# Performance work log

Hardware: AMD Instinct MI355X
Metric: run time of the kernel (lower is better)

Reference implementation:

```python
import jax, jax.numpy as jnp
import numpy as np

B, T, L = 4096, 26, 4      # batch, num sparse tables, bag size (multi-hot)
N_ROWS, M = 100000, 64     # rows per table, embedding dim
LN_BOT = [13, 512, 256, 64]
LN_TOP = [415, 512, 256, 1]


def _mlp_params(key, ln):
    Ws, bs = [], []
    for i in range(len(ln) - 1):
        n, m = ln[i], ln[i + 1]
        key, k1, k2 = jax.random.split(key, 3)
        Ws.append(jax.random.normal(k1, (m, n), jnp.float32) * np.sqrt(2.0 / (m + n)))
        bs.append(jax.random.normal(k2, (m,), jnp.float32) * np.sqrt(1.0 / m))
    return Ws, bs


def setup_inputs() -> dict:
    key = jax.random.key(0)
    k_dense, k_idx, k_emb, k_bot, k_top = jax.random.split(key, 5)
    dense_x = jax.random.normal(k_dense, (B, LN_BOT[0]), jnp.float32)
    sparse_idx = jax.random.randint(k_idx, (B, T, L), 0, N_ROWS, jnp.int64 if jax.config.jax_enable_x64 else jnp.int32)
    # per-table uniform init U(-1/sqrt(n), 1/sqrt(n)); all tables same size -> stacked
    bound = np.sqrt(1.0 / N_ROWS)
    emb_tables = jax.random.uniform(k_emb, (T, N_ROWS, M), jnp.float32, -bound, bound)
    bw, bb = _mlp_params(k_bot, LN_BOT)
    tw, tb = _mlp_params(k_top, LN_TOP)
    return {
        "dense_x": dense_x, "sparse_idx": sparse_idx, "emb_tables": emb_tables,
        "bot_W0": bw[0], "bot_b0": bb[0], "bot_W1": bw[1], "bot_b1": bb[1],
        "bot_W2": bw[2], "bot_b2": bb[2],
        "top_W0": tw[0], "top_b0": tb[0], "top_W1": tw[1], "top_b1": tb[1],
        "top_W2": tw[2], "top_b2": tb[2],
    }


def _dlrm_forward(dense_x, sparse_idx, emb_tables, bot, top):
    # bottom MLP (all ReLU; sigmoid_layer index not hit for bottom)
    x = dense_x
    for W, b in bot:
        x = jax.nn.relu(x @ W.T + b)                       # [B, 64] at the end
    # apply_emb: per-table EmbeddingBag(mode='sum'): gather L rows, sum-pool
    # emb_tables: [T, N, M], sparse_idx: [B, T, L] -> E: [B, T, M]
    E = jax.vmap(lambda tab, ix: tab[ix].sum(axis=1), in_axes=(0, 1), out_axes=1)(
        emb_tables, sparse_idx)
    # dot interaction: concat bottom output with pooled embeddings
    Tcat = jnp.concatenate([x[:, None, :], E], axis=1)     # [B, T+1, M]
    Z = jnp.einsum("bim,bjm->bij", Tcat, Tcat)             # [B, T+1, T+1]
    li, lj = np.tril_indices(T + 1, k=-1)                  # strictly lower triangle
    Zflat = Z[:, li, lj]                                   # [B, (T+1)T/2]
    R = jnp.concatenate([x, Zflat], axis=1)                # [B, 415]
    # top MLP: ReLU hidden, Sigmoid on last layer
    h = R
    for i, (W, b) in enumerate(top):
        h = h @ W.T + b
        h = jax.nn.sigmoid(h) if i == len(top) - 1 else jax.nn.relu(h)
    return h                                               # [B, 1]


def reference(dense_x, sparse_idx, emb_tables,
              bot_W0, bot_b0, bot_W1, bot_b1, bot_W2, bot_b2,
              top_W0, top_b0, top_W1, top_b1, top_W2, top_b2):
    bot = [(bot_W0, bot_b0), (bot_W1, bot_b1), (bot_W2, bot_b2)]
    top = [(top_W0, top_b0), (top_W1, top_b1), (top_W2, top_b2)]
    return _dlrm_forward(dense_x, sparse_idx, emb_tables, bot, top)
```

## Files before the change

kernel.cpp:

```cpp
#include <hip/hip_runtime.h>
#include <hip/hip_bf16.h>
#include <cstddef>
#include <cstdint>

#define BATCH 4096
#define TT 26
#define LL 4
#define NROWS 100000
#define MM 64
#define RSTR 512

typedef __attribute__((ext_vector_type(8))) short bf16x8;
typedef __attribute__((ext_vector_type(4))) float f32x4;
typedef __attribute__((ext_vector_type(16))) float f32x16;

#define AS1 __attribute__((address_space(1)))
#define AS3 __attribute__((address_space(3)))

__device__ __forceinline__ void gload_lds16(const void* g, void* l) {
    __builtin_amdgcn_global_load_lds((const AS1 unsigned int*)g,
                                     (AS3 unsigned int*)l, 16, 0, 0);
}

__device__ __forceinline__ float bu2f(unsigned short u) {
    unsigned int x = (unsigned int)u << 16;
    float f; __builtin_memcpy(&f, &x, 4); return f;
}

#define CONV_BLOCKS 2112
__global__ __launch_bounds__(256) void prep_kernel(
    const float* __restrict__ dense, const float* __restrict__ bw0,
    const float* __restrict__ bb0,
    const float* __restrict__ bw1, const float* __restrict__ bw2,
    const float* __restrict__ tw0, const float* __restrict__ tw1,
    __hip_bfloat16* __restrict__ x1,
    __hip_bfloat16* __restrict__ bw1b, __hip_bfloat16* __restrict__ bw2b,
    __hip_bfloat16* __restrict__ tw0b, __hip_bfloat16* __restrict__ tw1b)
{
    __shared__ float xr[13];
    if (blockIdx.x < CONV_BLOCKS) {
        int i = blockIdx.x * 256 + threadIdx.x;
        if (i < 131072) {
            bw1b[i] = __float2bfloat16(bw1[i]);
        } else if (i < 147456) {
            int j = i - 131072; bw2b[j] = __float2bfloat16(bw2[j]);
        } else if (i < 409600) {
            int j = i - 147456; int n = j >> 9, k = j & 511;
            tw0b[j] = __float2bfloat16(k < 415 ? tw0[n * 415 + k] : 0.f);
        } else {
            int j = i - 409600; tw1b[j] = __float2bfloat16(tw1[j]);
        }
        return;
    }
    int b = blockIdx.x - CONV_BLOCKS;
    if (threadIdx.x < 13) xr[threadIdx.x] = dense[b * 13 + threadIdx.x];
    __syncthreads();
    for (int j = threadIdx.x; j < 512; j += 256) {
        const float* w = bw0 + j * 13;
        float s = bb0[j];
#pragma unroll
        for (int k = 0; k < 13; k++) s = fmaf(xr[k], w[k], s);
        x1[(size_t)b * 512 + j] = __float2bfloat16(fmaxf(s, 0.f));
    }
}

template<int KK, int ACT>
__global__ __launch_bounds__(256) void gemm_fullk(
    const __hip_bfloat16* __restrict__ A,
    const __hip_bfloat16* __restrict__ W,
    const float* __restrict__ bias,
    __hip_bfloat16* __restrict__ C, int ldc)
{
    constexpr int HS   = KK / 2;
    constexpr int CPRH = KK / 16;
    constexpr int NI   = (64 * CPRH) / 256;
    __shared__ __align__(16) short As0[64 * HS];
    __shared__ __align__(16) short As1[64 * HS];
    __shared__ __align__(16) short Bs0[64 * HS];
    __shared__ __align__(16) short Bs1[64 * HS];

    const int tid  = threadIdx.x;
    const int lane = tid & 63;
    const int wid  = tid >> 6;
    const int wr   = wid >> 1, wc = wid & 1;

    const char* Ab = (const char*)A + (size_t)blockIdx.x * (64 * KK * 2);
    const char* Wb = (const char*)W + (size_t)blockIdx.y * (64 * KK * 2);

    auto stage = [&](const char* Gb, short* Ls, int h) {
#pragma unroll
        for (int j = 0; j < NI; j++) {
            int ci  = j * 256 + tid;
            int row = ci / CPRH;
            int cb  = (ci & (CPRH - 1)) * 16;
            int src = row * (2 * KK) + h * KK + (cb ^ ((row & 7) << 4));
            gload_lds16(Gb + src, (char*)Ls + row * KK + cb);
        }
    };
    stage(Ab, As0, 0); stage(Wb, Bs0, 0);
    stage(Ab, As1, 1); stage(Wb, Bs1, 1);

    const int frow = lane & 15;
    const int fkb  = (lane >> 4) * 16;
    const int xr   = (frow & 7) << 4;
    const int oA0  = (wr * 32 + frow) * KK;
    const int oA1  = oA0 + 16 * KK;
    const int oB0  = (wc * 32 + frow) * KK;
    const int oB1  = oB0 + 16 * KK;

    f32x4 acc[2][2] = {};

    auto compute = [&](const short* Ah, const short* Bh) {
#pragma unroll
        for (int ks = 0; ks < KK / 64; ks++) {
            int pc = (ks * 64 + fkb) ^ xr;
            bf16x8 a0 = *(const bf16x8*)((const char*)Ah + oA0 + pc);
            bf16x8 a1 = *(const bf16x8*)((const char*)Ah + oA1 + pc);
            bf16x8 b0 = *(const bf16x8*)((const char*)Bh + oB0 + pc);
            bf16x8 b1 = *(const bf16x8*)((const char*)Bh + oB1 + pc);
            acc[0][0] = __builtin_amdgcn_mfma_f32_16x16x32_bf16(a0, b0, acc[0][0], 0, 0, 0);
            acc[0][1] = __builtin_amdgcn_mfma_f32_16x16x32_bf16(a0, b1, acc[0][1], 0, 0, 0);
            acc[1][0] = __builtin_amdgcn_mfma_f32_16x16x32_bf16(a1, b0, acc[1][0], 0, 0, 0);
            acc[1][1] = __builtin_amdgcn_mfma_f32_16x16x32_bf16(a1, b1, acc[1][1], 0, 0, 0);
        }
    };

    asm volatile("s_waitcnt vmcnt(%0)" :: "i"(2 * NI) : "memory");
    __builtin_amdgcn_sched_barrier(0);
    __builtin_amdgcn_s_barrier();
    __builtin_amdgcn_sched_barrier(0);
    compute(As0, Bs0);
    asm volatile("s_waitcnt vmcnt(0)" ::: "memory");
    __builtin_amdgcn_sched_barrier(0);
    __builtin_amdgcn_s_barrier();
    __builtin_amdgcn_sched_barrier(0);
    compute(As1, Bs1);

    const int col0 = blockIdx.y * 64 + wc * 32 + (lane & 15);
    const int row0 = blockIdx.x * 64 + wr * 32 + (lane >> 4) * 4;
    float bias_n0 = bias[col0];
    float bias_n1 = bias[col0 + 16];
#pragma unroll
    for (int mi = 0; mi < 2; mi++) {
#pragma unroll
        for (int j = 0; j < 4; j++) {
            int row = row0 + mi * 16 + j;
            float v0 = acc[mi][0][j] + bias_n0;
            float v1 = acc[mi][1][j] + bias_n1;
            if (ACT == 1) { v0 = fmaxf(v0, 0.f); v1 = fmaxf(v1, 0.f); }
            C[(size_t)row * ldc + col0]      = __float2bfloat16(v0);
            C[(size_t)row * ldc + col0 + 16] = __float2bfloat16(v1);
        }
    }
}

__global__ __launch_bounds__(256) void embed_interact_kernel(
    const int* __restrict__ idx, const float* __restrict__ emb,
    __hip_bfloat16* __restrict__ R)
{
    __shared__ __align__(16) short T[32 * 64];
    __shared__ int sidx[TT * LL];
    const int b = blockIdx.x;
    const int tid = threadIdx.x;
    const int lane = tid & 63;
    const int w = tid >> 6;

    if (tid < TT * LL) sidx[tid] = idx[(size_t)b * (TT * LL) + tid];
    for (int i = tid; i < 5 * 64; i += 256) {
        int r = 27 + (i >> 6), l = i & 63;
        *(short*)((char*)T + r * 128 + ((l * 2) ^ ((r & 7) << 4))) = 0;
    }
    __syncthreads();

    float v[7][4];
#pragma unroll
    for (int rr = 0; rr < 7; rr++) {
        const int r = rr * 4 + w;
        if (r == 0) {
            v[rr][0] = __bfloat162float(R[(size_t)b * RSTR + lane]);
            v[rr][1] = 0.f; v[rr][2] = 0.f; v[rr][3] = 0.f;
        } else if (r < 27) {
            const int t = r - 1;
            const float* tab = emb + (size_t)t * NROWS * MM + lane;
#pragma unroll
            for (int l = 0; l < LL; l++)
                v[rr][l] = tab[(size_t)sidx[t * LL + l] * MM];
        }
    }
#pragma unroll
    for (int rr = 0; rr < 7; rr++) {
        const int r = rr * 4 + w;
        if (r < 27) {
            float s = v[rr][0] + v[rr][1] + v[rr][2] + v[rr][3];
            __hip_bfloat16 hv = __float2bfloat16(s);
            *(short*)((char*)T + r * 128 + ((lane * 2) ^ ((r & 7) << 4))) = *(short*)&hv;
        }
    }
    __syncthreads();

    __hip_bfloat16* Rb = R + (size_t)b * RSTR;
    if (w == 1) {
        Rb[415 + lane] = __float2bfloat16(0.f);
        if (lane < 33) Rb[479 + lane] = __float2bfloat16(0.f);
    }
    if (w == 0) {
        f32x16 acc = {};
#pragma unroll
        for (int m = 0; m < 4; m++) {
            int byteoff = (lane & 31) * 128 +
                          ((m * 32 + (lane >> 5) * 16) ^ ((lane & 7) << 4));
            bf16x8 f = *(const bf16x8*)((const char*)T + byteoff);
            acc = __builtin_amdgcn_mfma_f32_32x32x16_bf16(f, f, acc, 0, 0, 0);
        }
        const int col = lane & 31;
#pragma unroll
        for (int q = 0; q < 4; q++) {
#pragma unroll
            for (int j = 0; j < 4; j++) {
                int row = j + 8 * q + 4 * (lane >> 5);
                if (row < 27 && col < row)
                    Rb[64 + row * (row - 1) / 2 + col] = __float2bfloat16(acc[q * 4 + j]);
            }
        }
    }
}

__global__ __launch_bounds__(256) void top2_kernel(
    const __hip_bfloat16* __restrict__ h, const float* __restrict__ W,
    const float* __restrict__ bias, float* __restrict__ out)
{
    __shared__ float ws[256];
    int tid = threadIdx.x;
    ws[tid] = W[tid];
    __syncthreads();
    int b = blockIdx.x * 4 + (tid >> 6);
    int lane = tid & 63;
    const unsigned short* hb = (const unsigned short*)(h + (size_t)b * 256);
    ushort4 hv = *(const ushort4*)&hb[lane * 4];
    float4 wv = *(const float4*)&ws[lane * 4];
    float s = bu2f(hv.x) * wv.x + bu2f(hv.y) * wv.y + bu2f(hv.z) * wv.z + bu2f(hv.w) * wv.w;
#pragma unroll
    for (int off = 32; off >= 1; off >>= 1)
        s += __shfl_xor(s, off, 64);
    if (lane == 0) {
        float v = s + bias[0];
        out[b] = 1.0f / (1.0f + expf(-v));
    }
}

extern "C" void kernel_launch(void* const* d_in, const int* in_sizes, int n_in,
                              void* d_out, int out_size, void* d_ws, size_t ws_size,
                              hipStream_t stream) {
    const float* dense = (const float*)d_in[0];
    const int*   sidx  = (const int*)d_in[1];
    const float* emb   = (const float*)d_in[2];
    const float* bw0   = (const float*)d_in[3];
    const float* bb0   = (const float*)d_in[4];
    const float* bw1   = (const float*)d_in[5];
    const float* bb1   = (const float*)d_in[6];
    const float* bw2   = (const float*)d_in[7];
    const float* bb2   = (const float*)d_in[8];
    const float* tw0   = (const float*)d_in[9];
    const float* tb0   = (const float*)d_in[10];
    const float* tw1   = (const float*)d_in[11];
    const float* tb1   = (const float*)d_in[12];
    const float* tw2   = (const float*)d_in[13];
    const float* tb2   = (const float*)d_in[14];
    float* out = (float*)d_out;

    char* wsb = (char*)d_ws;
    __hip_bfloat16* x1   = (__hip_bfloat16*)(wsb);
    __hip_bfloat16* x2   = (__hip_bfloat16*)(wsb + (4u << 20));
    __hip_bfloat16* R    = (__hip_bfloat16*)(wsb + (8u << 20));
    __hip_bfloat16* h1   = (__hip_bfloat16*)(wsb + (12u << 20));
    __hip_bfloat16* h2   = (__hip_bfloat16*)(wsb + (16u << 20));
    __hip_bfloat16* bw1b = (__hip_bfloat16*)(wsb + (18u << 20));
    __hip_bfloat16* bw2b = bw1b + 131072;
    __hip_bfloat16* tw0b = bw2b + 16384;
    __hip_bfloat16* tw1b = tw0b + 262144;

    prep_kernel<<<CONV_BLOCKS + BATCH, 256, 0, stream>>>(
        dense, bw0, bb0, bw1, bw2, tw0, tw1, x1, bw1b, bw2b, tw0b, tw1b);

    gemm_fullk<512, 1><<<dim3(64, 4), 256, 0, stream>>>(x1, bw1b, bb1, x2, 256);

    gemm_fullk<256, 1><<<dim3(64, 1), 256, 0, stream>>>(x2, bw2b, bb2, R, RSTR);

    embed_interact_kernel<<<BATCH, 256, 0, stream>>>(sidx, emb, R);

    gemm_fullk<512, 1><<<dim3(64, 8), 256, 0, stream>>>(R, tw0b, tb0, h1, 512);

    gemm_fullk<512, 1><<<dim3(64, 4), 256, 0, stream>>>(h1, tw1b, tb1, h2, 256);

    top2_kernel<<<BATCH / 4, 256, 0, stream>>>(h2, tw2, tb2, out);
}
```

Baseline: 54.66 us.

## Fuse bottom MLP into one kernel, move embedding gather into prep kernel

The embedding gather now runs inside the weight-conversion prep kernel and writes pooled bf16 embeddings to a workspace buffer. All three bottom-MLP layers are fused into one kernel that processes 16 rows per block, keeping activations in LDS and using MFMA, which removes two GEMM launches and the x1/x2 round trips. A separate interaction kernel then handles four samples per block, one per wave. The aim is fewer launches and less intermediate traffic, at the cost of an extra E buffer round trip and a bottom MLP that runs on only 256 blocks.

After: 61.00 us. +11.6%, slower.

```diff
diff --git a/kernel.cpp b/kernel.cpp
--- a/kernel.cpp
+++ b/kernel.cpp
@@ -27,19 +27,19 @@
     float f; __builtin_memcpy(&f, &x, 4); return f;
 }
 
-#define CONV_BLOCKS 2112
-__global__ __launch_bounds__(256) void prep_kernel(
-    const float* __restrict__ dense, const float* __restrict__ bw0,
-    const float* __restrict__ bb0,
+#define CONVB 2112
+__global__ __launch_bounds__(256) void gather_conv_kernel(
+    const int* __restrict__ idx, const float* __restrict__ emb,
     const float* __restrict__ bw1, const float* __restrict__ bw2,
     const float* __restrict__ tw0, const float* __restrict__ tw1,
-    __hip_bfloat16* __restrict__ x1,
     __hip_bfloat16* __restrict__ bw1b, __hip_bfloat16* __restrict__ bw2b,
-    __hip_bfloat16* __restrict__ tw0b, __hip_bfloat16* __restrict__ tw1b)
-{
-    __shared__ float xr[13];
-    if (blockIdx.x < CONV_BLOCKS) {
-        int i = blockIdx.x * 256 + threadIdx.x;
+    __hip_bfloat16* __restrict__ tw0b, __hip_bfloat16* __restrict__ tw1b,
+    unsigned short* __restrict__ E)
+{
+    __shared__ int sidx[TT * LL];
+    const int tid = threadIdx.x;
+    if (blockIdx.x < CONVB) {
+        int i = blockIdx.x * 256 + tid;
         if (i < 131072) {
             bw1b[i] = __float2bfloat16(bw1[i]);
         } else if (i < 147456) {
@@ -52,16 +52,170 @@
         }
         return;
     }
-    int b = blockIdx.x - CONV_BLOCKS;
-    if (threadIdx.x < 13) xr[threadIdx.x] = dense[b * 13 + threadIdx.x];
-    __syncthreads();
-    for (int j = threadIdx.x; j < 512; j += 256) {
-        const float* w = bw0 + j * 13;
-        float s = bb0[j];
-#pragma unroll
-        for (int k = 0; k < 13; k++) s = fmaf(xr[k], w[k], s);
-        x1[(size_t)b * 512 + j] = __float2bfloat16(fmaxf(s, 0.f));
-    }
+    const int b = blockIdx.x - CONVB;
+    const int lane = tid & 63;
+    const int w = tid >> 6;
+    if (tid < TT * LL) sidx[tid] = idx[(size_t)b * (TT * LL) + tid];
+    __syncthreads();
+
+    float v[7][4];
+#pragma unroll
+    for (int rr = 0; rr < 7; rr++) {
+        int t = rr * 4 + w;
+        if (t < TT) {
+            const float* tab = emb + (size_t)t * NROWS * MM + lane;
+#pragma unroll
+            for (int l = 0; l < LL; l++)
+                v[rr][l] = tab[(size_t)sidx[t * LL + l] * MM];
+        }
+    }
+#pragma unroll
+    for (int rr = 0; rr < 7; rr++) {
+        int t = rr * 4 + w;
+        if (t < TT) {
+            float s = v[rr][0] + v[rr][1] + v[rr][2] + v[rr][3];
+            __hip_bfloat16 hv = __float2bfloat16(s);
+            E[(size_t)b * (TT * MM) + t * MM + lane] = *(unsigned short*)&hv;
+        }
+    }
+}
+
+__global__ __launch_bounds__(256) void bottom_mlp_kernel(
+    const float* __restrict__ dense, const float* __restrict__ bw0,
+    const float* __restrict__ bb0,
+    const __hip_bfloat16* __restrict__ w1b, const float* __restrict__ bb1,
+    const __hip_bfloat16* __restrict__ w2b, const float* __restrict__ bb2,
+    __hip_bfloat16* __restrict__ R)
+{
+    __shared__ float W0f[512 * 13];
+    __shared__ float dL[16 * 13];
+    __shared__ __align__(16) char x1L[16 * 1024];
+    __shared__ __align__(16) char x2L[16 * 512];
+    const int tid = threadIdx.x;
+    const int lane = tid & 63;
+    const int w = tid >> 6;
+    const int b0 = blockIdx.x * 16;
+
+    for (int i = tid; i < 512 * 13; i += 256) W0f[i] = bw0[i];
+    if (tid < 208) dL[tid] = dense[(size_t)b0 * 13 + tid];
+    __syncthreads();
+
+    {
+        const int m = tid & 15;
+        float dv[13];
+#pragma unroll
+        for (int k = 0; k < 13; k++) dv[k] = dL[m * 13 + k];
+#pragma unroll
+        for (int j = 0; j < 32; j++) {
+            int n = (tid >> 4) + j * 16;
+            float s = bb0[n];
+#pragma unroll
+            for (int k = 0; k < 13; k++) s = fmaf(dv[k], W0f[n * 13 + k], s);
+            __hip_bfloat16 hv = __float2bfloat16(fmaxf(s, 0.f));
+            *(short*)(x1L + m * 1024 + ((n * 2) ^ ((m & 7) << 4))) = *(short*)&hv;
+        }
+    }
+    __syncthreads();
+
+    const int fr = lane & 15;
+    const int fh = lane >> 4;
+
+    {
+        f32x4 acc1[4] = {};
+#pragma unroll
+        for (int kf = 0; kf < 16; kf++) {
+            bf16x8 af = *(const bf16x8*)(x1L + fr * 1024 + ((kf * 64 + fh * 16) ^ ((fr & 7) << 4)));
+#pragma unroll
+            for (int nf = 0; nf < 4; nf++) {
+                int n = w * 64 + nf * 16 + fr;
+                bf16x8 bf = *(const bf16x8*)((const short*)w1b + (size_t)n * 512 + kf * 32 + fh * 8);
+                acc1[nf] = __builtin_amdgcn_mfma_f32_16x16x32_bf16(af, bf, acc1[nf], 0, 0, 0);
+            }
+        }
+#pragma unroll
+        for (int nf = 0; nf < 4; nf++) {
+            int n = w * 64 + nf * 16 + fr;
+            float bias = bb1[n];
+#pragma unroll
+            for (int j = 0; j < 4; j++) {
+                int m = fh * 4 + j;
+                __hip_bfloat16 hv = __float2bfloat16(fmaxf(acc1[nf][j] + bias, 0.f));
+                *(short*)(x2L + m * 512 + ((n * 2) ^ ((m & 7) << 4))) = *(short*)&hv;
+            }
+        }
+    }
+    __syncthreads();
+
+    {
+        f32x4 acc2 = {};
+#pragma unroll
+        for (int kf = 0; kf < 8; kf++) {
+            bf16x8 af = *(const bf16x8*)(x2L + fr * 512 + ((kf * 64 + fh * 16) ^ ((fr & 7) << 4)));
+            bf16x8 bf = *(const bf16x8*)((const short*)w2b + (size_t)(w * 16 + fr) * 256 + kf * 32 + fh * 8);
+            acc2 = __builtin_amdgcn_mfma_f32_16x16x32_bf16(af, bf, acc2, 0, 0, 0);
+        }
+        int col = w * 16 + fr;
+        float bias = bb2[col];
+#pragma unroll
+        for (int j = 0; j < 4; j++) {
+            int m = fh * 4 + j;
+            R[(size_t)(b0 + m) * RSTR + col] = __float2bfloat16(fmaxf(acc2[j] + bias, 0.f));
+        }
+    }
+}
+
+__global__ __launch_bounds__(256) void interact_kernel(
+    const unsigned short* __restrict__ E, __hip_bfloat16* __restrict__ R)
+{
+    __shared__ __align__(16) char T[4][32 * 128];
+    const int tid = threadIdx.x;
+    const int lane = tid & 63;
+    const int w = tid >> 6;
+    const int b = blockIdx.x * 4 + w;
+    char* Tw = T[w];
+    const unsigned short* Eb = E + (size_t)b * (TT * MM);
+    const unsigned short* Xb = (const unsigned short*)R + (size_t)b * RSTR;
+
+#pragma unroll
+    for (int i = 0; i < 7; i++) {
+        int id = i * 64 + lane;
+        if (id < 432) {
+            int r = id >> 4, c4 = (id & 15) * 4;
+            const unsigned short* src = (r == 0) ? (Xb + c4) : (Eb + (r - 1) * 64 + c4);
+            ushort4 val = *(const ushort4*)src;
+            *(ushort4*)(Tw + r * 128 + ((c4 * 2) ^ ((r & 7) << 4))) = val;
+        }
+    }
+#pragma unroll
+    for (int i = 0; i < 2; i++) {
+        int id = i * 64 + lane;
+        if (id < 80) {
+            int r = 27 + (id >> 4), c4 = (id & 15) * 4;
+            *(ushort4*)(Tw + r * 128 + ((c4 * 2) ^ ((r & 7) << 4))) = (ushort4){0, 0, 0, 0};
+        }
+    }
+    __syncthreads();
+
+    f32x16 acc = {};
+#pragma unroll
+    for (int m = 0; m < 4; m++) {
+        int byteoff = (lane & 31) * 128 + ((m * 32 + (lane >> 5) * 16) ^ ((lane & 7) << 4));
+        bf16x8 f = *(const bf16x8*)(Tw + byteoff);
+        acc = __builtin_amdgcn_mfma_f32_32x32x16_bf16(f, f, acc, 0, 0, 0);
+    }
+    __hip_bfloat16* Rb = R + (size_t)b * RSTR;
+    const int col = lane & 31;
+#pragma unroll
+    for (int q = 0; q < 4; q++) {
+#pragma unroll
+        for (int j = 0; j < 4; j++) {
+            int row = j + 8 * q + 4 * (lane >> 5);
+            if (row < 27 && col < row)
+                Rb[64 + row * (row - 1) / 2 + col] = __float2bfloat16(acc[q * 4 + j]);
+        }
+    }
+    for (int p = lane; p < 97; p += 64)
+        Rb[415 + p] = __float2bfloat16(0.f);
 }
 
 template<int KK, int ACT>
@@ -150,77 +304,6 @@
             if (ACT == 1) { v0 = fmaxf(v0, 0.f); v1 = fmaxf(v1, 0.f); }
             C[(size_t)row * ldc + col0]      = __float2bfloat16(v0);
             C[(size_t)row * ldc + col0 + 16] = __float2bfloat16(v1);
-        }
-    }
-}
-
-__global__ __launch_bounds__(256) void embed_interact_kernel(
-    const int* __restrict__ idx, const float* __restrict__ emb,
-    __hip_bfloat16* __restrict__ R)
-{
-    __shared__ __align__(16) short T[32 * 64];
-    __shared__ int sidx[TT * LL];
-    const int b = blockIdx.x;
-    const int tid = threadIdx.x;
-    const int lane = tid & 63;
-    const int w = tid >> 6;
-
-    if (tid < TT * LL) sidx[tid] = idx[(size_t)b * (TT * LL) + tid];
-    for (int i = tid; i < 5 * 64; i += 256) {
-        int r = 27 + (i >> 6), l = i & 63;
-        *(short*)((char*)T + r * 128 + ((l * 2) ^ ((r & 7) << 4))) = 0;
-    }
-    __syncthreads();
-
-    float v[7][4];
-#pragma unroll
-    for (int rr = 0; rr < 7; rr++) {
-        const int r = rr * 4 + w;
-        if (r == 0) {
-            v[rr][0] = __bfloat162float(R[(size_t)b * RSTR + lane]);
-            v[rr][1] = 0.f; v[rr][2] = 0.f; v[rr][3] = 0.f;
-        } else if (r < 27) {
-            const int t = r - 1;
-            const float* tab = emb + (size_t)t * NROWS * MM + lane;
-#pragma unroll
-            for (int l = 0; l < LL; l++)
-                v[rr][l] = tab[(size_t)sidx[t * LL + l] * MM];
-        }
-    }
-#pragma unroll
-    for (int rr = 0; rr < 7; rr++) {
-        const int r = rr * 4 + w;
-        if (r < 27) {
-            float s = v[rr][0] + v[rr][1] + v[rr][2] + v[rr][3];
-            __hip_bfloat16 hv = __float2bfloat16(s);
-            *(short*)((char*)T + r * 128 + ((lane * 2) ^ ((r & 7) << 4))) = *(short*)&hv;
-        }
-    }
-    __syncthreads();
-
-    __hip_bfloat16* Rb = R + (size_t)b * RSTR;
-    if (w == 1) {
-        Rb[415 + lane] = __float2bfloat16(0.f);
-        if (lane < 33) Rb[479 + lane] = __float2bfloat16(0.f);
-    }
-    if (w == 0) {
-        f32x16 acc = {};
-#pragma unroll
-        for (int m = 0; m < 4; m++) {
-            int byteoff = (lane & 31) * 128 +
-                          ((m * 32 + (lane >> 5) * 16) ^ ((lane & 7) << 4));
-            bf16x8 f = *(const bf16x8*)((const char*)T + byteoff);
-            acc = __builtin_amdgcn_mfma_f32_32x32x16_bf16(f, f, acc, 0, 0, 0);
-        }
-        const int col = lane & 31;
-#pragma unroll
-        for (int q = 0; q < 4; q++) {
-#pragma unroll
-            for (int j = 0; j < 4; j++) {
-                int row = j + 8 * q + 4 * (lane >> 5);
-                if (row < 27 && col < row)
-                    Rb[64 + row * (row - 1) / 2 + col] = __float2bfloat16(acc[q * 4 + j]);
-            }
         }
     }
 }
@@ -269,24 +352,22 @@
     float* out = (float*)d_out;
 
     char* wsb = (char*)d_ws;
-    __hip_bfloat16* x1   = (__hip_bfloat16*)(wsb);
-    __hip_bfloat16* x2   = (__hip_bfloat16*)(wsb + (4u << 20));
-    __hip_bfloat16* R    = (__hip_bfloat16*)(wsb + (8u << 20));
-    __hip_bfloat16* h1   = (__hip_bfloat16*)(wsb + (12u << 20));
-    __hip_bfloat16* h2   = (__hip_bfloat16*)(wsb + (16u << 20));
-    __hip_bfloat16* bw1b = (__hip_bfloat16*)(wsb + (18u << 20));
+    unsigned short* E    = (unsigned short*)(wsb);
+    __hip_bfloat16* R    = (__hip_bfloat16*)(wsb + (16u << 20));
+    __hip_bfloat16* h1   = (__hip_bfloat16*)(wsb + (20u << 20));
+    __hip_bfloat16* h2   = (__hip_bfloat16*)(wsb + (24u << 20));
+    __hip_bfloat16* bw1b = (__hip_bfloat16*)(wsb + (26u << 20));
     __hip_bfloat16* bw2b = bw1b + 131072;
     __hip_bfloat16* tw0b = bw2b + 16384;
     __hip_bfloat16* tw1b = tw0b + 262144;
 
-    prep_kernel<<<CONV_BLOCKS + BATCH, 256, 0, stream>>>(
-        dense, bw0, bb0, bw1, bw2, tw0, tw1, x1, bw1b, bw2b, tw0b, tw1b);
-
-    gemm_fullk<512, 1><<<dim3(64, 4), 256, 0, stream>>>(x1, bw1b, bb1, x2, 256);
-
-    gemm_fullk<256, 1><<<dim3(64, 1), 256, 0, stream>>>(x2, bw2b, bb2, R, RSTR);
-
-    embed_interact_kernel<<<BATCH, 256, 0, stream>>>(sidx, emb, R);
+    gather_conv_kernel<<<CONVB + BATCH, 256, 0, stream>>>(
+        sidx, emb, bw1, bw2, tw0, tw1, bw1b, bw2b, tw0b, tw1b, E);
+
+    bottom_mlp_kernel<<<BATCH / 16, 256, 0, stream>>>(
+        dense, bw0, bb0, bw1b, bb1, bw2b, bb2, R);
+
+    interact_kernel<<<BATCH / 4, 256, 0, stream>>>(E, R);
 
     gemm_fullk<512, 1><<<dim3(64, 8), 256, 0, stream>>>(R, tw0b, tb0, h1, 512);
 
```
